# Performance work log

Hardware: AMD Instinct MI355X
Metric: run time of the kernel (lower is better)

## Reference

```python
import jax, jax.numpy as jnp
import numpy as np

B, T, D = 64, 4096, 100   # batch, tokens, token_dim == code_dim
K = 4                     # discrete_size: codebook entries
BETA = 0.25               # commitment loss weight


def setup_inputs() -> dict:
    key = jax.random.key(0)
    k_x, k_w, k_b, k_c = jax.random.split(key, 4)
    x = jax.random.normal(k_x, (B, T, D), dtype=jnp.float32)
    W1 = jax.random.normal(k_w, (D, D), dtype=jnp.float32) * (1.0 / np.sqrt(D))
    b1 = jax.random.normal(k_b, (D,), dtype=jnp.float32) * 0.01
    codebook = jax.random.normal(k_c, (K, D), dtype=jnp.float32)
    return {"x": x, "W1": W1, "b1": b1, "codebook": codebook, "quantize": 1}


def reference(x, W1, b1, codebook, quantize):
    # Linear1: Linear(100,100) + ReLU (torch Linear: x @ W.T + b)
    h = jax.nn.relu(jnp.einsum("btd,ed->bte", x, W1) + b1)  # [B,T,D]
    if not quantize:
        return (h, 0, 0, 0)
    # quantizer.compress: VQ-style cdist/argmin/straight-through/loss
    flat = h.reshape(-1, D)  # [N,D]
    d2 = (jnp.sum(flat * flat, axis=-1, keepdims=True)
          - 2.0 * flat @ codebook.T
          + jnp.sum(codebook * codebook, axis=-1))
    idx = jnp.argmin(d2, axis=-1)          # [N] nearest code indices
    q = codebook[idx]                       # [N,D] gathered codes
    sg = jax.lax.stop_gradient
    # codebook loss + commitment loss
    vq_loss = (jnp.mean((sg(flat) - q) ** 2)
               + BETA * jnp.mean((flat - sg(q)) ** 2))
    # straight-through quantized output
    aux = (flat + sg(q - flat)).reshape(B, T, D)
    payload = idx.reshape(B, T)
    return (h, payload, aux, vq_loss)
```

## Files before the change

### kernel.cpp

```cpp
#include <hip/hip_runtime.h>

#define D_DIM   100
#define K_CODES 4
#define RPB     64
#define TPB     256
#define PITCH   65
#define N_ROWS  262144
#define TAU     0.25
#define GEMM_TPB 512
#define GEMM_GRID 512
#define TILES_PER_WAVE 4
#define NB_PAD  112

typedef __attribute__((ext_vector_type(8))) __bf16 bf16x8;
typedef __attribute__((ext_vector_type(4))) float  f32x4;

__device__ __forceinline__ unsigned short f2bf_rne(float f) {
    unsigned int u = __builtin_bit_cast(unsigned int, f);
    unsigned int r = u + 0x7fffu + ((u >> 16) & 1u);
    return (unsigned short)(r >> 16);
}
__device__ __forceinline__ float bf2f(unsigned short b) {
    unsigned int u = ((unsigned int)b) << 16;
    return __builtin_bit_cast(float, u);
}

__global__ __launch_bounds__(GEMM_TPB, 4) void gemm_relu_mfma(
    const float* __restrict__ x, const float* __restrict__ W1,
    const float* __restrict__ b1, float* __restrict__ out_h)
{
    __shared__ unsigned short Bhi[NB_PAD * 128];
    __shared__ unsigned short Blo[NB_PAD * 128];
    const int tid  = threadIdx.x;
    const int lane = tid & 63;
    const int wave = tid >> 6;
    const int rw = lane & 15;
    const int kp = lane >> 4;

    for (int i = tid; i < NB_PAD * 128; i += GEMM_TPB) {
        int n = i >> 7, k = i & 127;
        float w = (n < D_DIM && k < D_DIM) ? W1[n * D_DIM + k] : 0.0f;
        unsigned short hb = f2bf_rne(w);
        unsigned short lb = f2bf_rne(w - bf2f(hb));
        int byte = (n * 256 + k * 2) ^ ((n & 7) << 4);
        *reinterpret_cast<unsigned short*>(reinterpret_cast<char*>(Bhi) + byte) = hb;
        *reinterpret_cast<unsigned short*>(reinterpret_cast<char*>(Blo) + byte) = lb;
    }

    float bias[7];
    #pragma unroll
    for (int ct = 0; ct < 7; ++ct) {
        int n = ct * 16 + rw;
        bias[ct] = (n < D_DIM) ? b1[n] : 0.0f;
    }

    __syncthreads();

    const int wg = blockIdx.x * 8 + wave;

    #pragma unroll
    for (int t = 0; t < TILES_PER_WAVE; ++t) {
        const int tile = wg + t * 4096;
        const float* base = x + (size_t)tile * 16 * D_DIM + rw * D_DIM;

        f32x4 f0[4], f1[4];
        #pragma unroll
        for (int kt = 0; kt < 3; ++kt) {
            const float* p = base + kt * 32 + kp * 8;
            f0[kt] = *reinterpret_cast<const f32x4*>(p);
            f1[kt] = *reinterpret_cast<const f32x4*>(p + 4);
        }
        if (kp == 0)
            f0[3] = *reinterpret_cast<const f32x4*>(base + 96);
        else
            f0[3] = (f32x4){0.f, 0.f, 0.f, 0.f};
        f1[3] = (f32x4){0.f, 0.f, 0.f, 0.f};

        bf16x8 ah[4], al[4];
        #pragma unroll
        for (int kt = 0; kt < 4; ++kt) {
            #pragma unroll
            for (int i = 0; i < 4; ++i) {
                __bf16 h0 = (__bf16)f0[kt][i];
                ah[kt][i] = h0;
                al[kt][i] = (__bf16)(f0[kt][i] - (float)h0);
                __bf16 h1 = (__bf16)f1[kt][i];
                ah[kt][4 + i] = h1;
                al[kt][4 + i] = (__bf16)(f1[kt][i] - (float)h1);
            }
        }

        const int rb = tile * 16 + kp * 4;
        const int n =  0;
        (void)n;
        #pragma unroll
        for (int ct = 0; ct < 7; ++ct) {
            const int col = ct * 16 + rw;
            bf16x8 bhf[4], blf[4];
            #pragma unroll
            for (int kt = 0; kt < 4; ++kt) {
                int byte = ((ct * 16 + rw) * 256 + (kt * 32 + kp * 8) * 2)
                           ^ (((ct * 16 + rw) & 7) << 4);
                bhf[kt] = *reinterpret_cast<const bf16x8*>(
                    reinterpret_cast<const char*>(Bhi) + byte);
                blf[kt] = *reinterpret_cast<const bf16x8*>(
                    reinterpret_cast<const char*>(Blo) + byte);
            }
            f32x4 a = {0.f, 0.f, 0.f, 0.f};
            #pragma unroll
            for (int kt = 0; kt < 4; ++kt) {
                a = __builtin_amdgcn_mfma_f32_16x16x32_bf16(ah[kt], blf[kt], a, 0, 0, 0);
                a = __builtin_amdgcn_mfma_f32_16x16x32_bf16(al[kt], bhf[kt], a, 0, 0, 0);
                a = __builtin_amdgcn_mfma_f32_16x16x32_bf16(ah[kt], bhf[kt], a, 0, 0, 0);
            }
            if (col < D_DIM) {
                #pragma unroll
                for (int i = 0; i < 4; ++i) {
                    float h = fmaxf(a[i] + bias[ct], 0.0f);
                    out_h[(size_t)(rb + i) * D_DIM + col] = h;
                }
            }
        }
    }
}

__global__ __launch_bounds__(TPB) void vq_kernel(
    const float* __restrict__ h, const float* __restrict__ x,
    const float* __restrict__ W1, const float* __restrict__ b1,
    const float* __restrict__ cb, const int* __restrict__ qflag,
    float* __restrict__ out_pay, float* __restrict__ out_aux,
    double* __restrict__ partials)
{
    __shared__ float  tile[D_DIM][PITCH];
    __shared__ double d2s[K_CODES][RPB];
    __shared__ int    idxs[RPB];
    __shared__ unsigned long long flagmask;
    const int tid  = threadIdx.x;
    const int lane = tid & 63;
    const int wave = tid >> 6;
    const int blk  = blockIdx.x;
    const int rowBase = blk * RPB;
    const int qz = *qflag;

    if (qz) {
        const float* hgc = h + (size_t)rowBase * D_DIM;
        for (int v = tid; v < (RPB * D_DIM) / 4; v += TPB) {
            float4 val = reinterpret_cast<const float4*>(hgc)[v];
            int r = v / 25;
            int d = (v % 25) * 4;
            tile[d + 0][r] = val.x; tile[d + 1][r] = val.y;
            tile[d + 2][r] = val.z; tile[d + 3][r] = val.w;
        }
        __syncthreads();
        {
            const int k = __builtin_amdgcn_readfirstlane(wave & 3);
            const float* crow = cb + k * D_DIM;
            double s = 0.0;
            #pragma unroll
            for (int d = 0; d < D_DIM; ++d) {
                double dh = (double)tile[d][lane] - (double)crow[d];
                s = fma(dh, dh, s);
            }
            d2s[k][lane] = s;
        }
        __syncthreads();

        if (wave == 0) {
            double best = d2s[0][lane], second = 1e300;
            int bi = 0;
            #pragma unroll
            for (int k = 1; k < K_CODES; ++k) {
                double v = d2s[k][lane];
                if (v < best) { second = best; best = v; bi = k; }
                else if (v < second) { second = v; }
            }
            idxs[lane] = bi;
            unsigned long long m = __ballot((second - best) < TAU);
            if (lane == 0) flagmask = m;
        }
        __syncthreads();

        {
            unsigned long long m = flagmask;
            int i = 0;
            while (m) {
                int r = __ffsll((long long)m) - 1;
                m &= m - 1;
                if ((i & 3) == wave) {
                    const int e1 = lane;
                    const int e2 = 64 + lane;
                    const bool has2 = (e2 < D_DIM);
                    float z1 = b1[e1];
                    float z2 = has2 ? b1[e2] : 0.0f;
                    const float* xr  = x + (size_t)(rowBase + r) * D_DIM;
                    const float* w1r = W1 + e1 * D_DIM;
                    const float* w2r = W1 + (has2 ? e2 : 0) * D_DIM;
                    #pragma unroll
                    for (int d4 = 0; d4 < 25; ++d4) {
                        float4 xv = reinterpret_cast<const float4*>(xr)[d4];
                        float4 wa = reinterpret_cast<const float4*>(w1r)[d4];
                        z1 = fmaf(xv.x, wa.x, z1); z1 = fmaf(xv.y, wa.y, z1);
                        z1 = fmaf(xv.z, wa.z, z1); z1 = fmaf(xv.w, wa.w, z1);
                        float4 wb = reinterpret_cast<const float4*>(w2r)[d4];
                        z2 = fmaf(xv.x, wb.x, z2); z2 = fmaf(xv.y, wb.y, z2);
                        z2 = fmaf(xv.z, wb.z, z2); z2 = fmaf(xv.w, wb.w, z2);
                    }
                    float h1 = fmaxf(z1, 0.0f);
                    float h2 = fmaxf(z2, 0.0f);
                    double dk[K_CODES];
                    #pragma unroll
                    for (int k = 0; k < K_CODES; ++k) {
                        double p;
                        {
                            double dh = (double)h1 - (double)cb[k * D_DIM + e1];
                            p = dh * dh;
                        }
                        if (has2) {
                            double dh = (double)h2 - (double)cb[k * D_DIM + e2];
                            p = fma(dh, dh, p);
                        }
                        for (int off = 32; off > 0; off >>= 1)
                            p += __shfl_down(p, off);
                        dk[k] = p;
                    }
                    if (lane == 0) {
                        double best = dk[0];
                        int bi = 0;
                        #pragma unroll
                        for (int k = 1; k < K_CODES; ++k)
                            if (dk[k] < best) { best = dk[k]; bi = k; }
                        idxs[r] = bi;
                    }
                }
                ++i;
            }
        }
        __syncthreads();

        if (wave == 0) {
            int bi = idxs[lane];
            out_pay[rowBase + lane] = (float)bi;
            double d2min = d2s[bi][lane];
            for (int off = 32; off > 0; off >>= 1)
                d2min += __shfl_down(d2min, off);
            if (lane == 0) partials[blk] = d2min;
        }

        float* ag = out_aux + (size_t)rowBase * D_DIM;
        for (int v = tid; v < (RPB * D_DIM) / 4; v += TPB) {
            int r = v / 25;
            int d = (v % 25) * 4;
            int bi = idxs[r];
            reinterpret_cast<float4*>(ag)[v] =
                reinterpret_cast<const float4*>(cb + bi * D_DIM + d)[0];
        }
    } else {
        if (wave == 0) {
            out_pay[rowBase + lane] = 0.0f;
            if (lane == 0) partials[blk] = 0.0;
        }
        float* ag = out_aux + (size_t)rowBase * D_DIM;
        for (int v = tid; v < (RPB * D_DIM) / 4; v += TPB)
            reinterpret_cast<float4*>(ag)[v] = make_float4(0, 0, 0, 0);
    }
}

__global__ __launch_bounds__(256) void vq_final_kernel(
    const double* __restrict__ partials, int n, float* __restrict__ loss_out)
{
    __shared__ double sm[256];
    int tid = threadIdx.x;
    double s = 0.0;
    for (int i = tid; i < n; i += 256) s += partials[i];
    sm[tid] = s;
    __syncthreads();
    for (int off = 128; off > 0; off >>= 1) {
        if (tid < off) sm[tid] += sm[tid + off];
        __syncthreads();
    }
    if (tid == 0) {
        double mse = sm[0] / ((double)N_ROWS * (double)D_DIM);
        loss_out[0] = (float)(1.25 * mse);
    }
}

extern "C" void kernel_launch(void* const* d_in, const int* in_sizes, int n_in,
                              void* d_out, int out_size, void* d_ws, size_t ws_size,
                              hipStream_t stream) {
    const float* x  = (const float*)d_in[0];
    const float* W1 = (const float*)d_in[1];
    const float* b1 = (const float*)d_in[2];
    const float* cb = (const float*)d_in[3];
    const int* qflag = (const int*)d_in[4];

    float* out = (float*)d_out;
    const int NR = in_sizes[0] / D_DIM;
    const int nblocks = NR / RPB;

    float* out_h    = out;
    float* out_pay  = out + (size_t)NR * D_DIM;
    float* out_aux  = out_pay + NR;
    float* out_loss = out_aux + (size_t)NR * D_DIM;
    double* partials = (double*)d_ws;

    gemm_relu_mfma<<<GEMM_GRID, GEMM_TPB, 0, stream>>>(x, W1, b1, out_h);
    vq_kernel<<<nblocks, TPB, 0, stream>>>(out_h, x, W1, b1, cb, qflag,
                                           out_pay, out_aux, partials);
    vq_final_kernel<<<1, 256, 0, stream>>>(partials, nblocks, out_loss);
}
```

Before: 117.9 us.

## Fuse VQ distance, argmin and aux write into the MFMA GEMM kernel

Merges the separate VQ kernel into the GEMM epilogue. Codebook distances are computed in fp32 straight from the MFMA accumulators and reduced with cross-lane shuffles, so h is no longer re-read from global memory through an LDS transpose. Rows whose best and second-best distances fall within a widened fp32 margin are recomputed exactly with an fp32 GEMV and fp64 distances. This removes one kernel launch and a full read of h, but adds register pressure and serialised per-wave fallback work, and the tile loop is no longer unrolled.

```diff
diff --git a/kernel.cpp b/kernel.cpp
--- a/kernel.cpp
+++ b/kernel.cpp
@@ -2,11 +2,8 @@
 
 #define D_DIM   100
 #define K_CODES 4
-#define RPB     64
-#define TPB     256
-#define PITCH   65
 #define N_ROWS  262144
-#define TAU     0.25
+#define TAU     0.5f
 #define GEMM_TPB 512
 #define GEMM_GRID 512
 #define TILES_PER_WAVE 4
@@ -25,9 +22,61 @@
     return __builtin_bit_cast(float, u);
 }
 
-__global__ __launch_bounds__(GEMM_TPB, 4) void gemm_relu_mfma(
+__device__ __forceinline__ int exact_row_argmin(
     const float* __restrict__ x, const float* __restrict__ W1,
-    const float* __restrict__ b1, float* __restrict__ out_h)
+    const float* __restrict__ b1, const float* __restrict__ cb,
+    int gr, int lane)
+{
+    const int e1 = lane;
+    const int e2 = 64 + lane;
+    const bool has2 = (e2 < D_DIM);
+    float z1 = b1[e1];
+    float z2 = has2 ? b1[e2] : 0.0f;
+    const float* xr  = x + (size_t)gr * D_DIM;
+    const float* w1r = W1 + e1 * D_DIM;
+    const float* w2r = W1 + (has2 ? e2 : 0) * D_DIM;
+    #pragma unroll
+    for (int d4 = 0; d4 < 25; ++d4) {
+        float4 xv = reinterpret_cast<const float4*>(xr)[d4];
+        float4 wa = reinterpret_cast<const float4*>(w1r)[d4];
+        z1 = fmaf(xv.x, wa.x, z1); z1 = fmaf(xv.y, wa.y, z1);
+        z1 = fmaf(xv.z, wa.z, z1); z1 = fmaf(xv.w, wa.w, z1);
+        float4 wb = reinterpret_cast<const float4*>(w2r)[d4];
+        z2 = fmaf(xv.x, wb.x, z2); z2 = fmaf(xv.y, wb.y, z2);
+        z2 = fmaf(xv.z, wb.z, z2); z2 = fmaf(xv.w, wb.w, z2);
+    }
+    float h1 = fmaxf(z1, 0.0f);
+    float h2 = fmaxf(z2, 0.0f);
+    double dk[K_CODES];
+    #pragma unroll
+    for (int k = 0; k < K_CODES; ++k) {
+        double p;
+        {
+            double dh = (double)h1 - (double)cb[k * D_DIM + e1];
+            p = dh * dh;
+        }
+        if (has2) {
+            double dh = (double)h2 - (double)cb[k * D_DIM + e2];
+            p = fma(dh, dh, p);
+        }
+        for (int off = 32; off > 0; off >>= 1)
+            p += __shfl_down(p, off);
+        dk[k] = p;
+    }
+    int bi_ex = 0;
+    double best = dk[0];
+    #pragma unroll
+    for (int k = 1; k < K_CODES; ++k)
+        if (dk[k] < best) { best = dk[k]; bi_ex = k; }
+    return __shfl(bi_ex, 0);
+}
+
+__global__ __launch_bounds__(GEMM_TPB, 4) void fused_gemm_vq(
+    const float* __restrict__ x, const float* __restrict__ W1,
+    const float* __restrict__ b1, const float* __restrict__ cb,
+    const int* __restrict__ qflag,
+    float* __restrict__ out_h, float* __restrict__ out_pay,
+    float* __restrict__ out_aux, double* __restrict__ partials)
 {
     __shared__ unsigned short Bhi[NB_PAD * 128];
     __shared__ unsigned short Blo[NB_PAD * 128];
@@ -46,19 +95,19 @@
         *reinterpret_cast<unsigned short*>(reinterpret_cast<char*>(Bhi) + byte) = hb;
         *reinterpret_cast<unsigned short*>(reinterpret_cast<char*>(Blo) + byte) = lb;
     }
-
     float bias[7];
     #pragma unroll
     for (int ct = 0; ct < 7; ++ct) {
         int n = ct * 16 + rw;
         bias[ct] = (n < D_DIM) ? b1[n] : 0.0f;
     }
-
+    const int qz = *qflag;
     __syncthreads();
 
     const int wg = blockIdx.x * 8 + wave;
-
-    #pragma unroll
+    double loss_acc = 0.0;
+
+    #pragma unroll 1
     for (int t = 0; t < TILES_PER_WAVE; ++t) {
         const int tile = wg + t * 4096;
         const float* base = x + (size_t)tile * 16 * D_DIM + rw * D_DIM;
@@ -91,16 +140,14 @@
         }
 
         const int rb = tile * 16 + kp * 4;
-        const int n =  0;
-        (void)n;
+        f32x4 acc[7];
         #pragma unroll
         for (int ct = 0; ct < 7; ++ct) {
             const int col = ct * 16 + rw;
             bf16x8 bhf[4], blf[4];
             #pragma unroll
             for (int kt = 0; kt < 4; ++kt) {
-                int byte = ((ct * 16 + rw) * 256 + (kt * 32 + kp * 8) * 2)
-                           ^ (((ct * 16 + rw) & 7) << 4);
+                int byte = (col * 256 + (kt * 32 + kp * 8) * 2) ^ ((col & 7) << 4);
                 bhf[kt] = *reinterpret_cast<const bf16x8*>(
                     reinterpret_cast<const char*>(Bhi) + byte);
                 blf[kt] = *reinterpret_cast<const bf16x8*>(
@@ -113,156 +160,113 @@
                 a = __builtin_amdgcn_mfma_f32_16x16x32_bf16(al[kt], bhf[kt], a, 0, 0, 0);
                 a = __builtin_amdgcn_mfma_f32_16x16x32_bf16(ah[kt], bhf[kt], a, 0, 0, 0);
             }
+            acc[ct] = a;
             if (col < D_DIM) {
                 #pragma unroll
+                for (int i = 0; i < 4; ++i)
+                    out_h[(size_t)(rb + i) * D_DIM + col] =
+                        fmaxf(a[i] + bias[ct], 0.0f);
+            }
+        }
+
+        if (qz) {
+            float s[4][K_CODES];
+            #pragma unroll
+            for (int i = 0; i < 4; ++i)
+                #pragma unroll
+                for (int k = 0; k < K_CODES; ++k) s[i][k] = 0.0f;
+            #pragma unroll
+            for (int ct = 0; ct < 7; ++ct) {
+                const int col = ct * 16 + rw;
+                float cc[K_CODES];
+                #pragma unroll
+                for (int k = 0; k < K_CODES; ++k)
+                    cc[k] = (col < D_DIM) ? cb[k * D_DIM + col] : 0.0f;
+                #pragma unroll
                 for (int i = 0; i < 4; ++i) {
-                    float h = fmaxf(a[i] + bias[ct], 0.0f);
-                    out_h[(size_t)(rb + i) * D_DIM + col] = h;
-                }
-            }
-        }
-    }
-}
-
-__global__ __launch_bounds__(TPB) void vq_kernel(
-    const float* __restrict__ h, const float* __restrict__ x,
-    const float* __restrict__ W1, const float* __restrict__ b1,
-    const float* __restrict__ cb, const int* __restrict__ qflag,
-    float* __restrict__ out_pay, float* __restrict__ out_aux,
-    double* __restrict__ partials)
-{
-    __shared__ float  tile[D_DIM][PITCH];
-    __shared__ double d2s[K_CODES][RPB];
-    __shared__ int    idxs[RPB];
-    __shared__ unsigned long long flagmask;
-    const int tid  = threadIdx.x;
-    const int lane = tid & 63;
-    const int wave = tid >> 6;
-    const int blk  = blockIdx.x;
-    const int rowBase = blk * RPB;
-    const int qz = *qflag;
-
-    if (qz) {
-        const float* hgc = h + (size_t)rowBase * D_DIM;
-        for (int v = tid; v < (RPB * D_DIM) / 4; v += TPB) {
-            float4 val = reinterpret_cast<const float4*>(hgc)[v];
-            int r = v / 25;
-            int d = (v % 25) * 4;
-            tile[d + 0][r] = val.x; tile[d + 1][r] = val.y;
-            tile[d + 2][r] = val.z; tile[d + 3][r] = val.w;
-        }
-        __syncthreads();
-        {
-            const int k = __builtin_amdgcn_readfirstlane(wave & 3);
-            const float* crow = cb + k * D_DIM;
-            double s = 0.0;
-            #pragma unroll
-            for (int d = 0; d < D_DIM; ++d) {
-                double dh = (double)tile[d][lane] - (double)crow[d];
-                s = fma(dh, dh, s);
-            }
-            d2s[k][lane] = s;
-        }
-        __syncthreads();
-
-        if (wave == 0) {
-            double best = d2s[0][lane], second = 1e300;
-            int bi = 0;
-            #pragma unroll
-            for (int k = 1; k < K_CODES; ++k) {
-                double v = d2s[k][lane];
-                if (v < best) { second = best; best = v; bi = k; }
-                else if (v < second) { second = v; }
-            }
-            idxs[lane] = bi;
-            unsigned long long m = __ballot((second - best) < TAU);
-            if (lane == 0) flagmask = m;
-        }
-        __syncthreads();
-
-        {
-            unsigned long long m = flagmask;
-            int i = 0;
-            while (m) {
-                int r = __ffsll((long long)m) - 1;
-                m &= m - 1;
-                if ((i & 3) == wave) {
-                    const int e1 = lane;
-                    const int e2 = 64 + lane;
-                    const bool has2 = (e2 < D_DIM);
-                    float z1 = b1[e1];
-                    float z2 = has2 ? b1[e2] : 0.0f;
-                    const float* xr  = x + (size_t)(rowBase + r) * D_DIM;
-                    const float* w1r = W1 + e1 * D_DIM;
-                    const float* w2r = W1 + (has2 ? e2 : 0) * D_DIM;
-                    #pragma unroll
-                    for (int d4 = 0; d4 < 25; ++d4) {
-                        float4 xv = reinterpret_cast<const float4*>(xr)[d4];
-                        float4 wa = reinterpret_cast<const float4*>(w1r)[d4];
-                        z1 = fmaf(xv.x, wa.x, z1); z1 = fmaf(xv.y, wa.y, z1);
-                        z1 = fmaf(xv.z, wa.z, z1); z1 = fmaf(xv.w, wa.w, z1);
-                        float4 wb = reinterpret_cast<const float4*>(w2r)[d4];
-                        z2 = fmaf(xv.x, wb.x, z2); z2 = fmaf(xv.y, wb.y, z2);
-                        z2 = fmaf(xv.z, wb.z, z2); z2 = fmaf(xv.w, wb.w, z2);
-                    }
-                    float h1 = fmaxf(z1, 0.0f);
-                    float h2 = fmaxf(z2, 0.0f);
-                    double dk[K_CODES];
+                    float h = fmaxf(acc[ct][i] + bias[ct], 0.0f);
                     #pragma unroll
                     for (int k = 0; k < K_CODES; ++k) {
-                        double p;
-                        {
-                            double dh = (double)h1 - (double)cb[k * D_DIM + e1];
-                            p = dh * dh;
-                        }
-                        if (has2) {
-                            double dh = (double)h2 - (double)cb[k * D_DIM + e2];
-                            p = fma(dh, dh, p);
-                        }
-                        for (int off = 32; off > 0; off >>= 1)
-                            p += __shfl_down(p, off);
-                        dk[k] = p;
+                        float e = h - cc[k];
+                        s[i][k] = fmaf(e, e, s[i][k]);
                     }
-                    if (lane == 0) {
-                        double best = dk[0];
-                        int bi = 0;
-                        #pragma unroll
-                        for (int k = 1; k < K_CODES; ++k)
-                            if (dk[k] < best) { best = dk[k]; bi = k; }
-                        idxs[r] = bi;
-                    }
-                }
-                ++i;
-            }
-        }
-        __syncthreads();
-
-        if (wave == 0) {
-            int bi = idxs[lane];
-            out_pay[rowBase + lane] = (float)bi;
-            double d2min = d2s[bi][lane];
-            for (int off = 32; off > 0; off >>= 1)
-                d2min += __shfl_down(d2min, off);
-            if (lane == 0) partials[blk] = d2min;
-        }
-
-        float* ag = out_aux + (size_t)rowBase * D_DIM;
-        for (int v = tid; v < (RPB * D_DIM) / 4; v += TPB) {
-            int r = v / 25;
-            int d = (v % 25) * 4;
-            int bi = idxs[r];
-            reinterpret_cast<float4*>(ag)[v] =
-                reinterpret_cast<const float4*>(cb + bi * D_DIM + d)[0];
-        }
-    } else {
-        if (wave == 0) {
-            out_pay[rowBase + lane] = 0.0f;
-            if (lane == 0) partials[blk] = 0.0;
-        }
-        float* ag = out_aux + (size_t)rowBase * D_DIM;
-        for (int v = tid; v < (RPB * D_DIM) / 4; v += TPB)
-            reinterpret_cast<float4*>(ag)[v] = make_float4(0, 0, 0, 0);
-    }
+                }
+            }
+            #pragma unroll
+            for (int off = 1; off < 16; off <<= 1)
+                #pragma unroll
+                for (int i = 0; i < 4; ++i)
+                    #pragma unroll
+                    for (int k = 0; k < K_CODES; ++k)
+                        s[i][k] += __shfl_xor(s[i][k], off);
+
+            int bi[4];
+            int flg[4];
+            #pragma unroll
+            for (int i = 0; i < 4; ++i) {
+                float best = s[i][0], second = 3.4e38f;
+                int b = 0;
+                #pragma unroll
+                for (int k = 1; k < K_CODES; ++k) {
+                    float v = s[i][k];
+                    if (v < best) { second = best; best = v; b = k; }
+                    else if (v < second) { second = v; }
+                }
+                bi[i] = b;
+                flg[i] = (second - best) < TAU;
+            }
+
+            #pragma unroll
+            for (int i = 0; i < 4; ++i) {
+                unsigned long long m = __ballot(flg[i] && rw == 0);
+                while (m) {
+                    int src = __ffsll((long long)m) - 1;
+                    m &= m - 1;
+                    int kpf = src >> 4;
+                    int gr = tile * 16 + kpf * 4 + i;
+                    int bx = exact_row_argmin(x, W1, b1, cb, gr, lane);
+                    if (kp == kpf) bi[i] = bx;
+                }
+            }
+
+            if (rw == 0) {
+                float4 pv = make_float4((float)bi[0], (float)bi[1],
+                                        (float)bi[2], (float)bi[3]);
+                *reinterpret_cast<float4*>(out_pay + tile * 16 + kp * 4) = pv;
+                #pragma unroll
+                for (int i = 0; i < 4; ++i)
+                    loss_acc += (double)s[i][bi[i]];
+            }
+
+            #pragma unroll
+            for (int ct = 0; ct < 7; ++ct) {
+                const int col = ct * 16 + rw;
+                if (col < D_DIM) {
+                    #pragma unroll
+                    for (int i = 0; i < 4; ++i)
+                        out_aux[(size_t)(rb + i) * D_DIM + col] =
+                            cb[bi[i] * D_DIM + col];
+                }
+            }
+        } else {
+            if (rw == 0)
+                *reinterpret_cast<float4*>(out_pay + tile * 16 + kp * 4) =
+                    make_float4(0.f, 0.f, 0.f, 0.f);
+            #pragma unroll
+            for (int ct = 0; ct < 7; ++ct) {
+                const int col = ct * 16 + rw;
+                if (col < D_DIM) {
+                    #pragma unroll
+                    for (int i = 0; i < 4; ++i)
+                        out_aux[(size_t)(rb + i) * D_DIM + col] = 0.0f;
+                }
+            }
+        }
+    }
+
+    for (int off = 32; off > 0; off >>= 1)
+        loss_acc += __shfl_down(loss_acc, off);
+    if (lane == 0) partials[wg] = loss_acc;
 }
 
 __global__ __launch_bounds__(256) void vq_final_kernel(
@@ -295,7 +299,6 @@
 
     float* out = (float*)d_out;
     const int NR = in_sizes[0] / D_DIM;
-    const int nblocks = NR / RPB;
 
     float* out_h    = out;
     float* out_pay  = out + (size_t)NR * D_DIM;
@@ -303,8 +306,7 @@
     float* out_loss = out_aux + (size_t)NR * D_DIM;
     double* partials = (double*)d_ws;
 
-    gemm_relu_mfma<<<GEMM_GRID, GEMM_TPB, 0, stream>>>(x, W1, b1, out_h);
-    vq_kernel<<<nblocks, TPB, 0, stream>>>(out_h, x, W1, b1, cb, qflag,
-                                           out_pay, out_aux, partials);
-    vq_final_kernel<<<1, 256, 0, stream>>>(partials, nblocks, out_loss);
-}
+    fused_gemm_vq<<<GEMM_GRID, GEMM_TPB, 0, stream>>>(
+        x, W1, b1, cb, qflag, out_h, out_pay, out_aux, partials);
+    vq_final_kernel<<<1, 256, 0, stream>>>(partials, GEMM_GRID * 8, out_loss);
+}
```

Result: slower. 299.3 us (+153.8%).
